# Kernel optimization log

Hardware: AMD Instinct MI355X
Metric: run time of the kernel (lower is better)

Reference implementation:

```python
import jax, jax.numpy as jnp
import numpy as np

D_MODEL = 512
N_HEADS = 8
D_K = D_MODEL // N_HEADS
MIN_LAG, MAX_LAG = 2, 12
N_LAGS = MAX_LAG - MIN_LAG + 1
SCALE = float(np.sqrt(D_K))


def setup_inputs() -> dict:
    key = jax.random.key(0)
    ks = jax.random.split(key, 6)
    B, T, N = 4, 128, 64
    w_scale = 1.0 / np.sqrt(D_MODEL)  # stable init like nn.Linear
    x = jax.random.normal(ks[0], (B, T, N, D_MODEL), dtype=jnp.float32)
    Wq = jax.random.normal(ks[1], (D_MODEL, D_MODEL), dtype=jnp.float32) * w_scale
    Wk = jax.random.normal(ks[2], (D_MODEL, D_MODEL), dtype=jnp.float32) * w_scale
    Wv = jax.random.normal(ks[3], (D_MODEL, D_MODEL), dtype=jnp.float32) * w_scale
    Wo = jax.random.normal(ks[4], (D_MODEL, D_MODEL), dtype=jnp.float32) * w_scale
    lag_emb = jax.random.normal(ks[5], (N_LAGS, D_MODEL), dtype=jnp.float32) * 0.02
    return {"x": x, "Wq": Wq, "Wk": Wk, "Wv": Wv, "Wo": Wo, "lag_emb": lag_emb}


def reference(x, Wq, Wk, Wv, Wo, lag_emb):
    B, T, N, D = x.shape
    # projections (torch Linear: y = x @ W.T), split heads
    q = (x @ Wq.T).reshape(B, T, N, N_HEADS, D_K)
    k = (x @ Wk.T).reshape(B, T, N, N_HEADS, D_K)
    v = (x @ Wv.T).reshape(B, T, N, N_HEADS, D_K)

    max_len = T - MIN_LAG  # longest valid lag-shifted window
    lag_outputs = []
    for lag_idx, lag in enumerate(range(MIN_LAG, MAX_LAG + 1)):
        if lag >= T:
            continue
        q_t = q[:, lag:]               # (B, T-lag, N, H, d_k)
        k_l = k[:, :-lag] + lag_emb[lag_idx].reshape(1, 1, 1, N_HEADS, D_K)
        v_l = v[:, :-lag]
        scores = jnp.einsum('btihc,btjhc->bthij', q_t, k_l) / SCALE
        attn = jax.nn.softmax(scores, axis=-1)  # dropout is identity at eval
        out = jnp.einsum('bthij,btjhc->btihc', attn, v_l)  # (B, T-lag, N, H, d_k)
        # pad time dim at the FRONT to max_len (matches F.pad(..., (..., max_len-L, 0)))
        pad_t = max_len - out.shape[1]
        out = jnp.pad(out, ((0, 0), (pad_t, 0), (0, 0), (0, 0), (0, 0)))
        lag_outputs.append(out)

    if not lag_outputs:
        return jnp.zeros_like(x)

    combined = jnp.stack(lag_outputs, axis=-1).mean(axis=-1)  # (B, max_len, N, H, d_k)
    combined = combined.reshape(B, max_len, N, D)
    if max_len < T:
        combined = jnp.pad(combined, ((0, 0), (T - max_len, 0), (0, 0), (0, 0)))
    output = combined @ Wo.T  # (B, T, N, D)
    return output
```

## Files before the change

### kernel.cpp

```cpp
#include <hip/hip_runtime.h>
#include <stdint.h>

typedef unsigned short u16;
typedef __attribute__((ext_vector_type(8))) short bf16x8;
typedef __attribute__((ext_vector_type(4))) float f32x4;
typedef __attribute__((ext_vector_type(4))) short short4v;
typedef __attribute__((ext_vector_type(8))) short short8v;
typedef __attribute__((ext_vector_type(4))) float float4v;

#define MFMA(a, b, c) __builtin_amdgcn_mfma_f32_16x16x32_bf16(a, b, c, 0, 0, 0)

__device__ __forceinline__ u16 f2bf(float f) {
  uint32_t u = __builtin_bit_cast(uint32_t, f);
  u += 0x7FFFu + ((u >> 16) & 1u);
  return (u16)(u >> 16);
}

__device__ __forceinline__ void load_lds16(const void* g, void* lds) {
  __builtin_amdgcn_global_load_lds((const __attribute__((address_space(1))) void*)g,
                                   (__attribute__((address_space(3))) void*)lds, 16, 0, 0);
}

struct CvtArgs {
  const float* src[5];
  u16* dst[5];
};

__global__ __launch_bounds__(256) void convert_kernel(CvtArgs a) {
  const size_t NX = 16777216u;
  const size_t NW = 262144u;
  size_t t8 = ((size_t)blockIdx.x * 256 + threadIdx.x) * 8;
  int seg;
  size_t off;
  if (t8 < NX) {
    seg = 0; off = t8;
  } else {
    size_t r = t8 - NX;
    seg = 1 + (int)(r >> 18);
    off = r & (NW - 1);
  }
  const float* s = a.src[seg] + off;
  u16* d = a.dst[seg] + off;
  float4v v0 = *((const float4v*)s);
  float4v v1 = *((const float4v*)(s + 4));
  short8v o;
  o[0] = (short)f2bf(v0[0]); o[1] = (short)f2bf(v0[1]);
  o[2] = (short)f2bf(v0[2]); o[3] = (short)f2bf(v0[3]);
  o[4] = (short)f2bf(v1[0]); o[5] = (short)f2bf(v1[1]);
  o[6] = (short)f2bf(v1[2]); o[7] = (short)f2bf(v1[3]);
  *((short8v*)d) = o;
}

template <int MODE>
__global__ __launch_bounds__(256) void gemm_bt(const u16* __restrict__ A,
                                               const u16* __restrict__ B,
                                               void* __restrict__ Cp) {
  __shared__ u16 lA[128 * 64];
  __shared__ u16 lB[128 * 64];
  const int tid = threadIdx.x;
  const int wave = tid >> 6, lane = tid & 63;
  const int g = lane >> 4, li = lane & 15;
  const int wr = wave >> 1, wc = wave & 1;
  const int m0 = blockIdx.x * 128, n0 = blockIdx.y * 128;
  const int rowa = tid >> 3, cl = tid & 7;

  f32x4 acc[4][4] = {};

  for (int kt = 0; kt < 8; ++kt) {
    __syncthreads();
#pragma unroll
    for (int it = 0; it < 4; ++it) {
      const int r = it * 32 + rowa;
      const int sc = (cl ^ (r & 7)) * 8;
      load_lds16(A + (size_t)(m0 + r) * 512 + kt * 64 + sc,
                 lA + (it * 256 + wave * 64) * 8);
      load_lds16(B + (size_t)(n0 + r) * 512 + kt * 64 + sc,
                 lB + (it * 256 + wave * 64) * 8);
    }
    __syncthreads();
#pragma unroll
    for (int ks = 0; ks < 2; ++ks) {
      bf16x8 af[4], bf[4];
#pragma unroll
      for (int mi = 0; mi < 4; ++mi) {
        const int r = wr * 64 + mi * 16 + li;
        af[mi] = *(const bf16x8*)(lA + r * 64 + (((ks * 4 + g) ^ (r & 7)) * 8));
      }
#pragma unroll
      for (int ni = 0; ni < 4; ++ni) {
        const int r = wc * 64 + ni * 16 + li;
        bf[ni] = *(const bf16x8*)(lB + r * 64 + (((ks * 4 + g) ^ (r & 7)) * 8));
      }
#pragma unroll
      for (int mi = 0; mi < 4; ++mi)
#pragma unroll
        for (int ni = 0; ni < 4; ++ni)
          acc[mi][ni] = MFMA(af[mi], bf[ni], acc[mi][ni]);
    }
  }

  if constexpr (MODE == 0) {
    u16* C = (u16*)Cp;
#pragma unroll
    for (int mi = 0; mi < 4; ++mi)
#pragma unroll
      for (int ni = 0; ni < 4; ++ni) {
        const int col = n0 + wc * 64 + ni * 16 + li;
        const int row0 = m0 + wr * 64 + mi * 16 + g * 4;
#pragma unroll
        for (int r = 0; r < 4; ++r)
          C[(size_t)(row0 + r) * 512 + col] = f2bf(acc[mi][ni][r]);
      }
  } else if constexpr (MODE == 1) {
    float* C = (float*)Cp;
#pragma unroll
    for (int mi = 0; mi < 4; ++mi)
#pragma unroll
      for (int ni = 0; ni < 4; ++ni) {
        const int col = n0 + wc * 64 + ni * 16 + li;
        const int row0 = m0 + wr * 64 + mi * 16 + g * 4;
#pragma unroll
        for (int r = 0; r < 4; ++r)
          C[(size_t)(row0 + r) * 512 + col] = acc[mi][ni][r];
      }
  } else {
    u16* C = (u16*)Cp;
#pragma unroll
    for (int mi = 0; mi < 4; ++mi)
#pragma unroll
      for (int ni = 0; ni < 4; ++ni) {
        const int col = n0 + wc * 64 + ni * 16 + li;
        const int hh = col >> 6, c = col & 63;
        const int row0 = m0 + wr * 64 + mi * 16 + g * 4;
        const int bt = row0 >> 6, n = row0 & 63;
        short4v pk;
#pragma unroll
        for (int r = 0; r < 4; ++r) pk[r] = (short)f2bf(acc[mi][ni][r]);
        *(short4v*)(C + ((size_t)bt * 8 + hh) * 4096 + (size_t)c * 64 + n) = pk;
      }
  }
}

__global__ __launch_bounds__(256) void attn_kernel(const u16* __restrict__ q,
                                                   const u16* __restrict__ k,
                                                   const u16* __restrict__ vt,
                                                   u16* __restrict__ Y) {
  __shared__ u16 pLds[4 * 64 * 64];
  const int tid = threadIdx.x;
  const int wave = tid >> 6, lane = tid & 63;
  const int g = lane >> 4, li = lane & 15;
  const int gid = blockIdx.x * 4 + wave;
  const int h = gid & 7, t = (gid >> 3) & 127, b = gid >> 10;
  u16* pw = pLds + wave * 4096;

  const size_t qoff = ((size_t)(b * 128 + t) * 64) * 512 + h * 64;
  bf16x8 qf[4][2];
#pragma unroll
  for (int fi = 0; fi < 4; ++fi)
#pragma unroll
    for (int ks = 0; ks < 2; ++ks)
      qf[fi][ks] = *(const bf16x8*)(q + qoff + (size_t)(fi * 16 + li) * 512 + ks * 32 + g * 8);

  f32x4 accO[4][4] = {};
  const int lmax = (t < 12) ? t : 12;
  for (int lag = 2; lag <= lmax; ++lag) {
    const int s = t - lag;
    const size_t koff = ((size_t)(b * 128 + s) * 64) * 512 + h * 64;
    bf16x8 kf[4][2];
#pragma unroll
    for (int fj = 0; fj < 4; ++fj)
#pragma unroll
      for (int ks = 0; ks < 2; ++ks)
        kf[fj][ks] = *(const bf16x8*)(k + koff + (size_t)(fj * 16 + li) * 512 + ks * 32 + g * 8);

    f32x4 S[4][4] = {};
#pragma unroll
    for (int ks = 0; ks < 2; ++ks)
#pragma unroll
      for (int fj = 0; fj < 4; ++fj)
#pragma unroll
        for (int fi = 0; fi < 4; ++fi)
          S[fj][fi] = MFMA(kf[fj][ks], qf[fi][ks], S[fj][fi]);

#pragma unroll
    for (int fi = 0; fi < 4; ++fi) {
      float m = S[0][fi][0];
#pragma unroll
      for (int fj = 0; fj < 4; ++fj)
#pragma unroll
        for (int r = 0; r < 4; ++r) m = fmaxf(m, S[fj][fi][r]);
      m = fmaxf(m, __shfl_xor(m, 16));
      m = fmaxf(m, __shfl_xor(m, 32));
      float sum = 0.f;
#pragma unroll
      for (int fj = 0; fj < 4; ++fj)
#pragma unroll
        for (int r = 0; r < 4; ++r) {
          float p = exp2f((S[fj][fi][r] - m) * 0.18033688011112f);
          S[fj][fi][r] = p;
          sum += p;
        }
      sum += __shfl_xor(sum, 16);
      sum += __shfl_xor(sum, 32);
      const float inv = 1.f / (11.f * sum);
#pragma unroll
      for (int fj = 0; fj < 4; ++fj)
#pragma unroll
        for (int r = 0; r < 4; ++r) S[fj][fi][r] *= inv;
    }

#pragma unroll
    for (int fj = 0; fj < 4; ++fj)
#pragma unroll
      for (int fi = 0; fi < 4; ++fi) {
        const int i = fi * 16 + li, j0 = fj * 16 + g * 4;
        short4v pk;
#pragma unroll
        for (int r = 0; r < 4; ++r) pk[r] = (short)f2bf(S[fj][fi][r]);
        const int chunk = (j0 >> 3) ^ (i & 7);
        *(short4v*)(pw + i * 64 + chunk * 8 + (j0 & 7)) = pk;
      }

    const size_t voff = ((size_t)(b * 128 + s) * 8 + h) * 4096;
    bf16x8 pf[4][2], vf[4][2];
#pragma unroll
    for (int mi = 0; mi < 4; ++mi)
#pragma unroll
      for (int ks = 0; ks < 2; ++ks) {
        const int i = mi * 16 + li;
        pf[mi][ks] = *(const bf16x8*)(pw + i * 64 + (((ks * 4 + g) ^ (i & 7)) * 8));
      }
#pragma unroll
    for (int fc = 0; fc < 4; ++fc)
#pragma unroll
      for (int ks = 0; ks < 2; ++ks)
        vf[fc][ks] = *(const bf16x8*)(vt + voff + (size_t)(fc * 16 + li) * 64 + ks * 32 + g * 8);
#pragma unroll
    for (int ks = 0; ks < 2; ++ks)
#pragma unroll
      for (int mi = 0; mi < 4; ++mi)
#pragma unroll
        for (int fc = 0; fc < 4; ++fc)
          accO[mi][fc] = MFMA(pf[mi][ks], vf[fc][ks], accO[mi][fc]);
  }

#pragma unroll
  for (int mi = 0; mi < 4; ++mi)
#pragma unroll
    for (int fc = 0; fc < 4; ++fc) {
      const int d = h * 64 + fc * 16 + li;
#pragma unroll
      for (int r = 0; r < 4; ++r) {
        const int i = mi * 16 + g * 4 + r;
        Y[((size_t)(b * 128 + t) * 64 + i) * 512 + d] = f2bf(accO[mi][fc][r]);
      }
    }
}

extern "C" void kernel_launch(void* const* d_in, const int* in_sizes, int n_in,
                              void* d_out, int out_size, void* d_ws, size_t ws_size,
                              hipStream_t stream) {
  (void)in_sizes; (void)n_in; (void)out_size; (void)ws_size;
  const float* x  = (const float*)d_in[0];
  const float* Wq = (const float*)d_in[1];
  const float* Wk = (const float*)d_in[2];
  const float* Wv = (const float*)d_in[3];
  const float* Wo = (const float*)d_in[4];

  u16* ws = (u16*)d_ws;
  const size_t NX = 16777216u, NW = 262144u;
  u16* xb  = ws;
  u16* wqb = xb + NX;
  u16* wkb = wqb + NW;
  u16* wvb = wkb + NW;
  u16* wob = wvb + NW;
  u16* qb  = wob + NW;
  u16* kb  = qb + NX;
  u16* vtb = kb + NX;
  u16* Yb  = xb;

  CvtArgs ca;
  ca.src[0] = x;  ca.dst[0] = xb;
  ca.src[1] = Wq; ca.dst[1] = wqb;
  ca.src[2] = Wk; ca.dst[2] = wkb;
  ca.src[3] = Wv; ca.dst[3] = wvb;
  ca.src[4] = Wo; ca.dst[4] = wob;
  convert_kernel<<<8704, 256, 0, stream>>>(ca);

  dim3 gg(256, 4);
  gemm_bt<0><<<gg, 256, 0, stream>>>(xb, wqb, qb);
  gemm_bt<0><<<gg, 256, 0, stream>>>(xb, wkb, kb);
  gemm_bt<2><<<gg, 256, 0, stream>>>(xb, wvb, vtb);

  attn_kernel<<<1024, 256, 0, stream>>>(qb, kb, vtb, Yb);

  gemm_bt<1><<<gg, 256, 0, stream>>>(Yb, wob, (float*)d_out);
}
```

Baseline: 304.2 us.

## Split lag loop across waves in attention kernel with LDS tree reduction

```diff
diff --git a/kernel.cpp b/kernel.cpp
--- a/kernel.cpp
+++ b/kernel.cpp
@@ -145,13 +145,15 @@
                                                    const u16* __restrict__ k,
                                                    const u16* __restrict__ vt,
                                                    u16* __restrict__ Y) {
-  __shared__ u16 pLds[4 * 64 * 64];
+  __shared__ __align__(16) char lds[34816];
   const int tid = threadIdx.x;
   const int wave = tid >> 6, lane = tid & 63;
   const int g = lane >> 4, li = lane & 15;
-  const int gid = blockIdx.x * 4 + wave;
-  const int h = gid & 7, t = (gid >> 3) & 127, b = gid >> 10;
-  u16* pw = pLds + wave * 4096;
+  const int bid = blockIdx.x;
+  const int h = bid & 7, t = (bid >> 3) & 127, b = bid >> 10;
+  u16* pw = (u16*)(lds + wave * 8192);
+  float* bufA = (float*)lds;
+  float* bufB = (float*)(lds + 17408);
 
   const size_t qoff = ((size_t)(b * 128 + t) * 64) * 512 + h * 64;
   bf16x8 qf[4][2];
@@ -163,7 +165,9 @@
 
   f32x4 accO[4][4] = {};
   const int lmax = (t < 12) ? t : 12;
-  for (int lag = 2; lag <= lmax; ++lag) {
+  for (int j = 0; j < 3; ++j) {
+    const int lag = 2 + wave + 4 * j;
+    if (lag > lmax) break;
     const int s = t - lag;
     const size_t koff = ((size_t)(b * 128 + s) * 64) * 512 + h * 64;
     bf16x8 kf[4][2];
@@ -244,17 +248,70 @@
           accO[mi][fc] = MFMA(pf[mi][ks], vf[fc][ks], accO[mi][fc]);
   }
 
-#pragma unroll
-  for (int mi = 0; mi < 4; ++mi)
-#pragma unroll
-    for (int fc = 0; fc < 4; ++fc) {
-      const int d = h * 64 + fc * 16 + li;
-#pragma unroll
-      for (int r = 0; r < 4; ++r) {
-        const int i = mi * 16 + g * 4 + r;
-        Y[((size_t)(b * 128 + t) * 64 + i) * 512 + d] = f2bf(accO[mi][fc][r]);
-      }
-    }
+  __syncthreads();
+  {
+    char* pa = (char*)bufA + lane * 272;
+    char* pb = (char*)bufB + lane * 272;
+    if (wave == 2) {
+#pragma unroll
+      for (int mi = 0; mi < 4; ++mi)
+#pragma unroll
+        for (int fc = 0; fc < 4; ++fc)
+          *(f32x4*)(pa + (mi * 4 + fc) * 16) = accO[mi][fc];
+    }
+    if (wave == 3) {
+#pragma unroll
+      for (int mi = 0; mi < 4; ++mi)
+#pragma unroll
+        for (int fc = 0; fc < 4; ++fc)
+          *(f32x4*)(pb + (mi * 4 + fc) * 16) = accO[mi][fc];
+    }
+    __syncthreads();
+    if (wave == 0) {
+#pragma unroll
+      for (int mi = 0; mi < 4; ++mi)
+#pragma unroll
+        for (int fc = 0; fc < 4; ++fc)
+          accO[mi][fc] += *(f32x4*)(pa + (mi * 4 + fc) * 16);
+    }
+    if (wave == 1) {
+#pragma unroll
+      for (int mi = 0; mi < 4; ++mi)
+#pragma unroll
+        for (int fc = 0; fc < 4; ++fc)
+          accO[mi][fc] += *(f32x4*)(pb + (mi * 4 + fc) * 16);
+    }
+    __syncthreads();
+    if (wave == 1) {
+#pragma unroll
+      for (int mi = 0; mi < 4; ++mi)
+#pragma unroll
+        for (int fc = 0; fc < 4; ++fc)
+          *(f32x4*)(pa + (mi * 4 + fc) * 16) = accO[mi][fc];
+    }
+    __syncthreads();
+    if (wave == 0) {
+#pragma unroll
+      for (int mi = 0; mi < 4; ++mi)
+#pragma unroll
+        for (int fc = 0; fc < 4; ++fc)
+          accO[mi][fc] += *(f32x4*)(pa + (mi * 4 + fc) * 16);
+    }
+  }
+
+  if (wave == 0) {
+#pragma unroll
+    for (int mi = 0; mi < 4; ++mi)
+#pragma unroll
+      for (int fc = 0; fc < 4; ++fc) {
+        const int d = h * 64 + fc * 16 + li;
+#pragma unroll
+        for (int r = 0; r < 4; ++r) {
+          const int i = mi * 16 + g * 4 + r;
+          Y[((size_t)(b * 128 + t) * 64 + i) * 512 + d] = f2bf(accO[mi][fc][r]);
+        }
+      }
+  }
 }
 
 extern "C" void kernel_launch(void* const* d_in, const int* in_sizes, int n_in,
@@ -292,7 +349,7 @@
   gemm_bt<0><<<gg, 256, 0, stream>>>(xb, wkb, kb);
   gemm_bt<2><<<gg, 256, 0, stream>>>(xb, wvb, vtb);
 
-  attn_kernel<<<1024, 256, 0, stream>>>(qb, kb, vtb, Yb);
+  attn_kernel<<<4096, 256, 0, stream>>>(qb, kb, vtb, Yb);
 
   gemm_bt<1><<<gg, 256, 0, stream>>>(Yb, wob, (float*)d_out);
 }
```

Measured after the change: 364.3 us. 19.7% more time.

## Split attention block across waves by query rows with double-buffered LDS K/V tiles

Applied to the files above, without the earlier changes.

```diff
diff --git a/kernel.cpp b/kernel.cpp
--- a/kernel.cpp
+++ b/kernel.cpp
@@ -145,116 +145,120 @@
                                                    const u16* __restrict__ k,
                                                    const u16* __restrict__ vt,
                                                    u16* __restrict__ Y) {
-  __shared__ u16 pLds[4 * 64 * 64];
+  __shared__ __align__(16) char lds[40960];
   const int tid = threadIdx.x;
   const int wave = tid >> 6, lane = tid & 63;
   const int g = lane >> 4, li = lane & 15;
-  const int gid = blockIdx.x * 4 + wave;
-  const int h = gid & 7, t = (gid >> 3) & 127, b = gid >> 10;
-  u16* pw = pLds + wave * 4096;
-
-  const size_t qoff = ((size_t)(b * 128 + t) * 64) * 512 + h * 64;
-  bf16x8 qf[4][2];
-#pragma unroll
-  for (int fi = 0; fi < 4; ++fi)
-#pragma unroll
-    for (int ks = 0; ks < 2; ++ks)
-      qf[fi][ks] = *(const bf16x8*)(q + qoff + (size_t)(fi * 16 + li) * 512 + ks * 32 + g * 8);
-
-  f32x4 accO[4][4] = {};
+  const int bid = blockIdx.x;
+  const int h = bid & 7, t = (bid >> 3) & 127, b = bid >> 10;
+  char* pbuf = lds + 32768 + wave * 2048;
+  const int i0 = wave * 16;
+  const int sub = lane >> 3, cl = lane & 7;
+  const int slot0 = wave * 4;
+
+  const size_t qoff = ((size_t)((b * 128 + t) * 64 + i0 + li)) * 512 + h * 64;
+  bf16x8 qf[2];
+#pragma unroll
+  for (int ks = 0; ks < 2; ++ks)
+    qf[ks] = *(const bf16x8*)(q + qoff + ks * 32 + g * 8);
+
+  f32x4 accO[4] = {};
   const int lmax = (t < 12) ? t : 12;
-  for (int lag = 2; lag <= lmax; ++lag) {
-    const int s = t - lag;
-    const size_t koff = ((size_t)(b * 128 + s) * 64) * 512 + h * 64;
-    bf16x8 kf[4][2];
-#pragma unroll
-    for (int fj = 0; fj < 4; ++fj)
+
+  auto stage = [&](int st, int cur) {
+    char* base = lds + cur * 16384;
+    const size_t koff = ((size_t)((b * 128 + st) * 64)) * 512 + h * 64;
+    const size_t voff = ((size_t)((b * 128 + st) * 8 + h)) * 4096;
+#pragma unroll
+    for (int m = 0; m < 4; ++m) {
+      const int slot = slot0 + m;
+      if (slot < 8) {
+        const int j = slot * 8 + sub;
+        load_lds16(k + koff + (size_t)j * 512 + (cl ^ (j & 7)) * 8,
+                   base + slot * 1024);
+      } else {
+        const int c = (slot - 8) * 8 + sub;
+        load_lds16(vt + voff + c * 64 + (cl ^ (c & 7)) * 8,
+                   base + 8192 + (slot - 8) * 1024);
+      }
+    }
+  };
+
+  if (lmax >= 2) {
+    stage(t - 2, 0);
+    int cur = 0;
+    for (int lag = 2; lag <= lmax; ++lag) {
+      __syncthreads();
+      if (lag < lmax) stage(t - lag - 1, cur ^ 1);
+
+      const u16* kt = (const u16*)(lds + cur * 16384);
+      const u16* vtile = kt + 4096;
+
+      f32x4 S[4] = {};
 #pragma unroll
       for (int ks = 0; ks < 2; ++ks)
-        kf[fj][ks] = *(const bf16x8*)(k + koff + (size_t)(fj * 16 + li) * 512 + ks * 32 + g * 8);
-
-    f32x4 S[4][4] = {};
-#pragma unroll
-    for (int ks = 0; ks < 2; ++ks)
+#pragma unroll
+        for (int fj = 0; fj < 4; ++fj) {
+          const int j = fj * 16 + li;
+          bf16x8 kfr = *(const bf16x8*)(kt + j * 64 + (((ks * 4 + g) ^ (j & 7)) * 8));
+          S[fj] = MFMA(kfr, qf[ks], S[fj]);
+        }
+
+      float mx = S[0][0];
 #pragma unroll
       for (int fj = 0; fj < 4; ++fj)
 #pragma unroll
-        for (int fi = 0; fi < 4; ++fi)
-          S[fj][fi] = MFMA(kf[fj][ks], qf[fi][ks], S[fj][fi]);
-
-#pragma unroll
-    for (int fi = 0; fi < 4; ++fi) {
-      float m = S[0][fi][0];
+        for (int r = 0; r < 4; ++r) mx = fmaxf(mx, S[fj][r]);
+      mx = fmaxf(mx, __shfl_xor(mx, 16));
+      mx = fmaxf(mx, __shfl_xor(mx, 32));
+      float sum = 0.f;
 #pragma unroll
       for (int fj = 0; fj < 4; ++fj)
 #pragma unroll
-        for (int r = 0; r < 4; ++r) m = fmaxf(m, S[fj][fi][r]);
-      m = fmaxf(m, __shfl_xor(m, 16));
-      m = fmaxf(m, __shfl_xor(m, 32));
-      float sum = 0.f;
-#pragma unroll
-      for (int fj = 0; fj < 4; ++fj)
-#pragma unroll
         for (int r = 0; r < 4; ++r) {
-          float p = exp2f((S[fj][fi][r] - m) * 0.18033688011112f);
-          S[fj][fi][r] = p;
+          float p = exp2f((S[fj][r] - mx) * 0.18033688011112f);
+          S[fj][r] = p;
           sum += p;
         }
       sum += __shfl_xor(sum, 16);
       sum += __shfl_xor(sum, 32);
       const float inv = 1.f / (11.f * sum);
-#pragma unroll
-      for (int fj = 0; fj < 4; ++fj)
-#pragma unroll
-        for (int r = 0; r < 4; ++r) S[fj][fi][r] *= inv;
-    }
-
-#pragma unroll
-    for (int fj = 0; fj < 4; ++fj)
-#pragma unroll
-      for (int fi = 0; fi < 4; ++fi) {
-        const int i = fi * 16 + li, j0 = fj * 16 + g * 4;
+
+#pragma unroll
+      for (int fj = 0; fj < 4; ++fj) {
+        const int j0 = fj * 16 + g * 4;
         short4v pk;
 #pragma unroll
-        for (int r = 0; r < 4; ++r) pk[r] = (short)f2bf(S[fj][fi][r]);
-        const int chunk = (j0 >> 3) ^ (i & 7);
-        *(short4v*)(pw + i * 64 + chunk * 8 + (j0 & 7)) = pk;
-      }
-
-    const size_t voff = ((size_t)(b * 128 + s) * 8 + h) * 4096;
-    bf16x8 pf[4][2], vf[4][2];
-#pragma unroll
-    for (int mi = 0; mi < 4; ++mi)
-#pragma unroll
-      for (int ks = 0; ks < 2; ++ks) {
-        const int i = mi * 16 + li;
-        pf[mi][ks] = *(const bf16x8*)(pw + i * 64 + (((ks * 4 + g) ^ (i & 7)) * 8));
-      }
-#pragma unroll
-    for (int fc = 0; fc < 4; ++fc)
+        for (int r = 0; r < 4; ++r) pk[r] = (short)f2bf(S[fj][r] * inv);
+        const int chunk = (j0 >> 3) ^ (li & 7);
+        *(short4v*)(pbuf + li * 128 + chunk * 16 + (j0 & 7) * 2) = pk;
+      }
+
+      bf16x8 pf[2];
 #pragma unroll
       for (int ks = 0; ks < 2; ++ks)
-        vf[fc][ks] = *(const bf16x8*)(vt + voff + (size_t)(fc * 16 + li) * 64 + ks * 32 + g * 8);
-#pragma unroll
-    for (int ks = 0; ks < 2; ++ks)
-#pragma unroll
-      for (int mi = 0; mi < 4; ++mi)
-#pragma unroll
-        for (int fc = 0; fc < 4; ++fc)
-          accO[mi][fc] = MFMA(pf[mi][ks], vf[fc][ks], accO[mi][fc]);
-  }
-
-#pragma unroll
-  for (int mi = 0; mi < 4; ++mi)
-#pragma unroll
-    for (int fc = 0; fc < 4; ++fc) {
-      const int d = h * 64 + fc * 16 + li;
-#pragma unroll
-      for (int r = 0; r < 4; ++r) {
-        const int i = mi * 16 + g * 4 + r;
-        Y[((size_t)(b * 128 + t) * 64 + i) * 512 + d] = f2bf(accO[mi][fc][r]);
-      }
-    }
+        pf[ks] = *(const bf16x8*)(pbuf + li * 128 + (((ks * 4 + g) ^ (li & 7)) * 16));
+#pragma unroll
+      for (int ks = 0; ks < 2; ++ks)
+#pragma unroll
+        for (int fc = 0; fc < 4; ++fc) {
+          const int c = fc * 16 + li;
+          bf16x8 vfr = *(const bf16x8*)(vtile + c * 64 + (((ks * 4 + g) ^ (c & 7)) * 8));
+          accO[fc] = MFMA(pf[ks], vfr, accO[fc]);
+        }
+      cur ^= 1;
+    }
+  }
+
+#pragma unroll
+  for (int fc = 0; fc < 4; ++fc) {
+    const int d = h * 64 + fc * 16 + li;
+#pragma unroll
+    for (int r = 0; r < 4; ++r) {
+      const int i = i0 + g * 4 + r;
+      Y[((size_t)((b * 128 + t) * 64 + i)) * 512 + d] = f2bf(accO[fc][r]);
+    }
+  }
 }
 
 extern "C" void kernel_launch(void* const* d_in, const int* in_sizes, int n_in,
@@ -292,7 +296,7 @@
   gemm_bt<0><<<gg, 256, 0, stream>>>(xb, wkb, kb);
   gemm_bt<2><<<gg, 256, 0, stream>>>(xb, wvb, vtb);
 
-  attn_kernel<<<1024, 256, 0, stream>>>(qb, kb, vtb, Yb);
+  attn_kernel<<<4096, 256, 0, stream>>>(qb, kb, vtb, Yb);
 
   gemm_bt<1><<<gg, 256, 0, stream>>>(Yb, wob, (float*)d_out);
 }
```

New measurement: 251.4 us. -17.4%, faster.
